# Optimization experiments

Hardware: AMD Instinct MI355X
Metric: run time of the kernel (lower is better)

The kernel has to match this reference:

```python
import jax, jax.numpy as jnp
import numpy as np
from jax import lax

K_SIZE = 5  # dilated_kernel_size


def dcls_kernel(w, p, k=K_SIZE):
    """Build dense (Cout,Cin,k,k) kernel from DCLS v1 bilinear interpolation.
    w: (Cout,Cin,Kc) weights; p: (2,Cout,Cin,Kc) learnable positions."""
    lim = k // 2
    pos = jnp.clip(p, -lim, lim) + lim          # in [0, k-1]
    i = jnp.floor(pos).astype(jnp.int32)
    r = pos - i                                  # bilinear fractions
    Co, Ci, Kc = w.shape
    co = jnp.arange(Co)[:, None, None]
    ci = jnp.arange(Ci)[None, :, None]
    i1, i2 = i[0], i[1]
    r1, r2 = r[0], r[1]
    # scatter into (k+1)x(k+1) grid so i+1 never goes out of bounds, then trim
    K = jnp.zeros((Co, Ci, k + 1, k + 1), w.dtype)
    K = K.at[co, ci, i1,     i2    ].add(w * (1 - r1) * (1 - r2))
    K = K.at[co, ci, i1 + 1, i2    ].add(w * r1 * (1 - r2))
    K = K.at[co, ci, i1,     i2 + 1].add(w * (1 - r1) * r2)
    K = K.at[co, ci, i1 + 1, i2 + 1].add(w * r1 * r2)
    return K[:, :, :k, :k]


def conv2d(x, K, pad):
    return lax.conv_general_dilated(
        x, K, window_strides=(1, 1), padding=[(pad, pad), (pad, pad)],
        dimension_numbers=('NCHW', 'OIHW', 'NCHW'))


def maxpool2(x):
    return lax.reduce_window(x, -jnp.inf, lax.max, (1, 1, 2, 2), (1, 1, 2, 2), 'VALID')


def setup_inputs() -> dict:
    key = jax.random.key(0)
    ks = jax.random.split(key, 12)
    lim = K_SIZE // 2
    B = 4096
    x = jax.random.normal(ks[0], (B, 1, 28, 28), jnp.float32)
    w1 = jax.random.normal(ks[1], (32, 1, 16), jnp.float32) * 0.2
    p1 = jax.random.uniform(ks[2], (2, 32, 1, 16), jnp.float32, -lim, lim)
    b1 = jnp.zeros((32,), jnp.float32)
    w2 = jax.random.normal(ks[3], (64, 32, 32), jnp.float32) * 0.05
    p2 = jax.random.uniform(ks[4], (2, 64, 32, 32), jnp.float32, -lim, lim)
    b2 = jnp.zeros((64,), jnp.float32)
    fc1_w = jax.random.normal(ks[5], (128, 64 * 7 * 7), jnp.float32) * 0.02
    fc1_b = jnp.zeros((128,), jnp.float32)
    fc2_w = jax.random.normal(ks[6], (10, 128), jnp.float32) * 0.08
    fc2_b = jnp.zeros((10,), jnp.float32)
    return dict(x=x, w1=w1, p1=p1, b1=b1, w2=w2, p2=p2, b2=b2,
                fc1_w=fc1_w, fc1_b=fc1_b, fc2_w=fc2_w, fc2_b=fc2_b)


def reference(x, w1, p1, b1, w2, p2, b2, fc1_w, fc1_b, fc2_w, fc2_b):
    h = conv2d(x, dcls_kernel(w1, p1), pad=2) + b1[None, :, None, None]
    h = maxpool2(jax.nn.relu(h))                       # (B,32,14,14)
    h = conv2d(h, dcls_kernel(w2, p2), pad=2) + b2[None, :, None, None]
    h = maxpool2(jax.nn.relu(h))                       # (B,64,7,7)
    h = h.reshape(-1, 64 * 7 * 7)
    h = jax.nn.relu(h @ fc1_w.T + fc1_b)
    return h @ fc2_w.T + fc2_b                         # (B,10)
```

## Files before the change

kernel.cpp:

```cpp
#include <hip/hip_runtime.h>
#include <hip/hip_bf16.h>

typedef __attribute__((ext_vector_type(8))) short short8;
typedef __attribute__((ext_vector_type(4))) short short4v;
typedef __attribute__((ext_vector_type(4))) float float4v;

static __device__ __forceinline__ unsigned short f2bf(float f) {
    unsigned u = __float_as_uint(f);
    unsigned r = (u + 0x7FFF + ((u >> 16) & 1)) >> 16;
    return (unsigned short)r;
}

__global__ __launch_bounds__(256) void prep_all(
    const float* __restrict__ w1, const float* __restrict__ p1,
    const float* __restrict__ w2, const float* __restrict__ p2,
    const float* __restrict__ fc1w,
    unsigned short* __restrict__ K1b,
    unsigned short* __restrict__ Kt,
    unsigned short* __restrict__ w1b) {
    const int blk = blockIdx.x;
    const int t = threadIdx.x;

    if (blk < 8) {
        int cell = blk * 256 + t;
        int co = cell >> 6;
        int k = cell & 63;
        int wr = k >> 3;
        int kx = k & 7;
        float acc = 0.f;
        if (wr < 5 && kx < 5) {
#pragma unroll 8
            for (int kc = 0; kc < 16; ++kc) {
                float wv = w1[co * 16 + kc];
                float pa = p1[co * 16 + kc];
                float pb = p1[512 + co * 16 + kc];
                float pos1 = fminf(fmaxf(pa, -2.f), 2.f) + 2.f;
                float pos2 = fminf(fmaxf(pb, -2.f), 2.f) + 2.f;
                int i1 = (int)floorf(pos1);
                int i2 = (int)floorf(pos2);
                float r1 = pos1 - (float)i1;
                float r2 = pos2 - (float)i2;
                float c = 0.f;
                if (i1 == wr && i2 == kx) c += (1.f - r1) * (1.f - r2);
                if (i1 + 1 == wr && i2 == kx) c += r1 * (1.f - r2);
                if (i1 == wr && i2 + 1 == kx) c += (1.f - r1) * r2;
                if (i1 + 1 == wr && i2 + 1 == kx) c += r1 * r2;
                acc += wv * c;
            }
        }
        K1b[cell] = f2bf(acc);
    } else if (blk < 208) {
        int cell = (blk - 8) * 256 + t;
        int kk = cell >> 11;
        int co = (cell >> 5) & 63;
        int ci = cell & 31;
        int ky = kk / 5;
        int kx = kk - 5 * ky;
        const int base = (co * 32 + ci) * 32;
        float acc = 0.f;
#pragma unroll 8
        for (int kc = 0; kc < 32; ++kc) {
            float wv = w2[base + kc];
            float pa = p2[base + kc];
            float pb = p2[65536 + base + kc];
            float pos1 = fminf(fmaxf(pa, -2.f), 2.f) + 2.f;
            float pos2 = fminf(fmaxf(pb, -2.f), 2.f) + 2.f;
            int i1 = (int)floorf(pos1);
            int i2 = (int)floorf(pos2);
            float r1 = pos1 - (float)i1;
            float r2 = pos2 - (float)i2;
            float c = 0.f;
            if (i1 == ky && i2 == kx) c += (1.f - r1) * (1.f - r2);
            if (i1 + 1 == ky && i2 == kx) c += r1 * (1.f - r2);
            if (i1 == ky && i2 + 1 == kx) c += (1.f - r1) * r2;
            if (i1 + 1 == ky && i2 + 1 == kx) c += r1 * r2;
            acc += wv * c;
        }
        Kt[cell] = f2bf(acc);
    } else {
        int i8 = ((blk - 208) * 256 + t) * 8;
        float4 v0 = *(const float4*)(fc1w + i8);
        float4 v1 = *(const float4*)(fc1w + i8 + 4);
        short8 o = {(short)f2bf(v0.x), (short)f2bf(v0.y), (short)f2bf(v0.z),
                    (short)f2bf(v0.w), (short)f2bf(v1.x), (short)f2bf(v1.y),
                    (short)f2bf(v1.z), (short)f2bf(v1.w)};
        *(short8*)(w1b + i8) = o;
    }
}

__global__ __launch_bounds__(256, 4) void fused_conv_mfma(
    const float* __restrict__ x,
    const unsigned short* __restrict__ K1b,
    const unsigned short* __restrict__ Kt,
    const float* __restrict__ b1,
    const float* __restrict__ b2,
    unsigned short* __restrict__ h2) {
    __shared__ __align__(16) unsigned short h1p[18 * 20 * 40];
    __shared__ __align__(16) unsigned short sm4[4 * 29 * 44];
    __shared__ __align__(16) unsigned short sm_xb[784];

    const int b = blockIdx.x;
    const int tid = threadIdx.x;
    const int lane = tid & 63;
    const int wv = tid >> 6;
    const int n16 = lane & 15;
    const int cig = lane >> 4;

    const int yi = 2 * (n16 >> 3) + ((n16 >> 1) & 1);
    const int xi = 2 * ((n16 >> 2) & 1) + (n16 & 1);
    const int pYo = cig >> 1, pXo = cig & 1;

    for (int t = tid; t < 1800; t += 256) ((uint4*)h1p)[t] = uint4{0, 0, 0, 0};
    {
        const float* xb = x + (size_t)b * 784;
        for (int t = tid; t < 784; t += 256) sm_xb[t] = f2bf(xb[t]);
    }
    __syncthreads();

    if (tid < 116) {
        int s = tid / 29;
        int r = tid - s * 29;
        unsigned short* dst = sm4 + (s * 29 + r) * 44;
        bool rok = r < 28;
#pragma unroll
        for (int g = 0; g < 11; ++g) {
            short4v v;
#pragma unroll
            for (int e = 0; e < 4; ++e) {
                int c = g * 4 + e + s - 4;
                v[e] = (short)((rok && (unsigned)c < 28u) ? sm_xb[r * 28 + c]
                                                          : (unsigned short)0);
            }
            *(short4v*)(dst + g * 4) = v;
        }
    }

    short8 bw[2][2];
    float bias1[2], bias2[4];
#pragma unroll
    for (int cot = 0; cot < 2; ++cot) {
#pragma unroll
        for (int h = 0; h < 2; ++h)
            bw[cot][h] = *(const short8*)(K1b + (cot * 16 + n16) * 64 + h * 32 + cig * 8);
        bias1[cot] = b1[cot * 16 + n16];
    }
#pragma unroll
    for (int cot = 0; cot < 4; ++cot) bias2[cot] = b2[cot * 16 + n16];

    const int s1 = (xi + 2) & 3;
    const int pb1 = (xi + 2) & ~3;
    const unsigned short* a1base = sm4 + s1 * (29 * 44) + pb1;

    __syncthreads();

    for (int i = 0; i < 13; ++i) {
        int t = wv + 4 * i;
        if (t < 49) {
            int tY = t / 7, tX = t - 7 * tY;
            const unsigned short* ab = a1base + 4 * tX;
            int r0 = 4 * tY + yi - 2 + cig;
            int r1 = r0 + 4;
            int rr0 = ((unsigned)r0 < 28u) ? r0 : 28;
            int rr1 = ((unsigned)r1 < 28u) ? r1 : 28;
            short4v lo0 = *(const short4v*)(ab + rr0 * 44);
            short4v hi0 = *(const short4v*)(ab + rr0 * 44 + 4);
            short4v lo1 = *(const short4v*)(ab + rr1 * 44);
            short4v hi1 = *(const short4v*)(ab + rr1 * 44 + 4);
            short8 af0 = {lo0[0], lo0[1], lo0[2], lo0[3], hi0[0], hi0[1], hi0[2], hi0[3]};
            short8 af1 = {lo1[0], lo1[1], lo1[2], lo1[3], hi1[0], hi1[1], hi1[2], hi1[3]};
            int pY = 2 * tY + pYo, pX = 2 * tX + pXo;
#pragma unroll
            for (int cot = 0; cot < 2; ++cot) {
                float4v acc = {0.f, 0.f, 0.f, 0.f};
                acc = __builtin_amdgcn_mfma_f32_16x16x32_bf16(af0, bw[cot][0], acc, 0, 0, 0);
                acc = __builtin_amdgcn_mfma_f32_16x16x32_bf16(af1, bw[cot][1], acc, 0, 0, 0);
                float v = fmaxf(fmaxf(acc[0], acc[1]), fmaxf(acc[2], acc[3]));
                v = fmaxf(v + bias1[cot], 0.f);
                h1p[((pY + 2) * 20 + (pX + 2)) * 40 + cot * 16 + n16] = f2bf(v);
            }
        }
    }
    __syncthreads();

    const unsigned short* Ab[4];
    int pY2[4], pX2[4];
#pragma unroll
    for (int i = 0; i < 4; ++i) {
        int t = wv * 4 + i;
        int tY = t >> 2, tX = t & 3;
        int y2 = 4 * tY + yi;
        y2 = (y2 > 13) ? 13 : y2;
        int x2 = 4 * tX + xi;
        Ab[i] = h1p + (y2 * 20 + x2) * 40 + cig * 8;
        pY2[i] = 2 * tY + pYo;
        pX2[i] = 2 * tX + pXo;
    }

    float4v acc[4][4];
#pragma unroll
    for (int i = 0; i < 4; ++i)
#pragma unroll
        for (int c = 0; c < 4; ++c) acc[i][c] = float4v{0.f, 0.f, 0.f, 0.f};

#pragma unroll
    for (int ky = 0; ky < 5; ++ky) {
#pragma unroll
        for (int kx = 0; kx < 5; ++kx) {
            int kk = ky * 5 + kx;
            short8 wf[4];
#pragma unroll
            for (int cot = 0; cot < 4; ++cot)
                wf[cot] = *(const short8*)(Kt + ((kk * 64 + cot * 16 + n16) * 32 + cig * 8));
#pragma unroll
            for (int i = 0; i < 4; ++i) {
                short8 af = *(const short8*)(Ab[i] + (ky * 20 + kx) * 40);
#pragma unroll
                for (int cot = 0; cot < 4; ++cot)
                    acc[i][cot] = __builtin_amdgcn_mfma_f32_16x16x32_bf16(
                        af, wf[cot], acc[i][cot], 0, 0, 0);
            }
        }
    }

    unsigned short* outb = h2 + (size_t)b * 3136;
#pragma unroll
    for (int i = 0; i < 4; ++i) {
        bool ok = (pY2[i] < 7) & (pX2[i] < 7);
#pragma unroll
        for (int cot = 0; cot < 4; ++cot) {
            float4v a = acc[i][cot];
            float v = fmaxf(fmaxf(a[0], a[1]), fmaxf(a[2], a[3]));
            v = fmaxf(v + bias2[cot], 0.f);
            if (ok)
                outb[(cot * 16 + n16) * 49 + pY2[i] * 7 + pX2[i]] = f2bf(v);
        }
    }
}

__global__ __launch_bounds__(256) void fc1_mfma(
    const unsigned short* __restrict__ A,
    const unsigned short* __restrict__ Wb,
    float* __restrict__ part, size_t PB) {
    const int blk = blockIdx.x;
    const int kh = blk % 7;
    const int m0 = (blk / 7) * 16;
    const int tid = threadIdx.x;
    const int wv = tid >> 6;
    const int lane = tid & 63;
    const int n16 = lane & 15;
    const int cig = lane >> 4;

    const unsigned short* Arow = A + (size_t)(m0 + n16) * 3136 + cig * 8 + kh * 448;
    const unsigned short* W0 = Wb + (size_t)(wv * 32 + n16) * 3136 + cig * 8 + kh * 448;
    const unsigned short* W1 = W0 + 16 * 3136;

    float4v acc0 = {0.f, 0.f, 0.f, 0.f};
    float4v acc1 = {0.f, 0.f, 0.f, 0.f};
#pragma unroll 7
    for (int k = 0; k < 448; k += 32) {
        short8 a = *(const short8*)(Arow + k);
        short8 w0 = *(const short8*)(W0 + k);
        short8 w1 = *(const short8*)(W1 + k);
        acc0 = __builtin_amdgcn_mfma_f32_16x16x32_bf16(a, w0, acc0, 0, 0, 0);
        acc1 = __builtin_amdgcn_mfma_f32_16x16x32_bf16(a, w1, acc1, 0, 0, 0);
    }
    float* o = part + (size_t)kh * PB;
#pragma unroll
    for (int r = 0; r < 4; ++r) {
        int row = m0 + cig * 4 + r;
        o[(size_t)row * 128 + wv * 32 + n16] = acc0[r];
        o[(size_t)row * 128 + wv * 32 + 16 + n16] = acc1[r];
    }
}

__global__ __launch_bounds__(256) void fc2_kernel(
    const float* __restrict__ part, size_t PB,
    const float* __restrict__ fc1b,
    const float* __restrict__ W, const float* __restrict__ bias,
    float* __restrict__ out, int total) {
    __shared__ float smW[10 * 132];
    __shared__ float smB1[128];
    __shared__ float smB[10];
    int t = threadIdx.x;
    for (int i = t; i < 1280; i += 256) {
        int n = i >> 7, k = i & 127;
        smW[n * 132 + k] = W[i];
    }
    if (t < 128) smB1[t] = fc1b[t];
    if (t < 10) smB[t] = bias[t];
    __syncthreads();
    int idx = blockIdx.x * 256 + t;
    if (idx < total) {
        int b = idx / 10;
        int n = idx - b * 10;
        const float4* bb = (const float4*)smB1;
        const float4* wr = (const float4*)(smW + n * 132);
        float acc = smB[n];
#pragma unroll 4
        for (int k = 0; k < 32; ++k) {
            float4 s = *(const float4*)(part + (size_t)b * 128 + 4 * k);
#pragma unroll
            for (int j = 1; j < 7; ++j) {
                float4 pj = *(const float4*)(part + (size_t)j * PB + (size_t)b * 128 + 4 * k);
                s.x += pj.x; s.y += pj.y; s.z += pj.z; s.w += pj.w;
            }
            float4 bv = bb[k];
            float4 w = wr[k];
            acc += fmaxf(s.x + bv.x, 0.f) * w.x + fmaxf(s.y + bv.y, 0.f) * w.y +
                   fmaxf(s.z + bv.z, 0.f) * w.z + fmaxf(s.w + bv.w, 0.f) * w.w;
        }
        out[idx] = acc;
    }
}

extern "C" void kernel_launch(void* const* d_in, const int* in_sizes, int n_in,
                              void* d_out, int out_size, void* d_ws, size_t ws_size,
                              hipStream_t stream) {
    const float* x    = (const float*)d_in[0];
    const float* w1   = (const float*)d_in[1];
    const float* p1   = (const float*)d_in[2];
    const float* b1   = (const float*)d_in[3];
    const float* w2   = (const float*)d_in[4];
    const float* p2   = (const float*)d_in[5];
    const float* b2   = (const float*)d_in[6];
    const float* fc1w = (const float*)d_in[7];
    const float* fc1b = (const float*)d_in[8];
    const float* fc2w = (const float*)d_in[9];
    const float* fc2b = (const float*)d_in[10];
    float* out = (float*)d_out;

    const int B = in_sizes[0] / 784;

    float* ws = (float*)d_ws;
    unsigned short* Kt  = (unsigned short*)ws;
    unsigned short* K1b = (unsigned short*)(ws + 25600);
    unsigned short* w1b = (unsigned short*)(ws + 26624);
    unsigned short* h2b = (unsigned short*)(ws + 227328);
    float* fc1p = ws + 227328 + (size_t)B * 1568;

    prep_all<<<404, 256, 0, stream>>>(w1, p1, w2, p2, fc1w, K1b, Kt, w1b);
    fused_conv_mfma<<<B, 256, 0, stream>>>(x, K1b, Kt, b1, b2, h2b);
    fc1_mfma<<<(B / 16) * 7, 256, 0, stream>>>(h2b, w1b, fc1p, (size_t)B * 128);
    fc2_kernel<<<(B * 10 + 255) / 256, 256, 0, stream>>>(fc1p, (size_t)B * 128,
                                                         fc1b, fc2w, fc2b, out, B * 10);
}
```

Before: 257.5 us.

## Shrink conv LDS, retile conv2, LDS-tile fc1 over 64 rows, split fc2 reduction

The conv kernel trims its LDS buffers (tighter h1 padding, smaller shifted-input rows, input staged in the h1 buffer) to raise occupancy. It also remaps conv2 tiles so only 14 of 16 tile slots do MMA work, and reorders the conv1 weight layout to match. fc1 now stages 64 A rows in shared memory and reuses each weight fragment across 4 M-tiles, which cuts redundant global weight loads. fc2 splits each dot product across 4 lanes and combines them with shuffles for more parallelism. Together these touch every kernel and add index complexity that could introduce layout bugs.

```diff
diff --git a/kernel.cpp b/kernel.cpp
--- a/kernel.cpp
+++ b/kernel.cpp
@@ -23,12 +23,13 @@
 
     if (blk < 8) {
         int cell = blk * 256 + t;
-        int co = cell >> 6;
-        int k = cell & 63;
-        int wr = k >> 3;
+        int half = cell >> 10;
+        int co = (cell >> 5) & 31;
+        int k = cell & 31;
+        int ky = (k >> 3) + 4 * half;
         int kx = k & 7;
         float acc = 0.f;
-        if (wr < 5 && kx < 5) {
+        if (kx < 5 && ky < 5) {
 #pragma unroll 8
             for (int kc = 0; kc < 16; ++kc) {
                 float wv = w1[co * 16 + kc];
@@ -41,10 +42,10 @@
                 float r1 = pos1 - (float)i1;
                 float r2 = pos2 - (float)i2;
                 float c = 0.f;
-                if (i1 == wr && i2 == kx) c += (1.f - r1) * (1.f - r2);
-                if (i1 + 1 == wr && i2 == kx) c += r1 * (1.f - r2);
-                if (i1 == wr && i2 + 1 == kx) c += (1.f - r1) * r2;
-                if (i1 + 1 == wr && i2 + 1 == kx) c += r1 * r2;
+                if (i1 == ky && i2 == kx) c += (1.f - r1) * (1.f - r2);
+                if (i1 + 1 == ky && i2 == kx) c += r1 * (1.f - r2);
+                if (i1 == ky && i2 + 1 == kx) c += (1.f - r1) * r2;
+                if (i1 + 1 == ky && i2 + 1 == kx) c += r1 * r2;
                 acc += wv * c;
             }
         }
@@ -95,9 +96,8 @@
     const float* __restrict__ b1,
     const float* __restrict__ b2,
     unsigned short* __restrict__ h2) {
-    __shared__ __align__(16) unsigned short h1p[18 * 20 * 40];
-    __shared__ __align__(16) unsigned short sm4[4 * 29 * 44];
-    __shared__ __align__(16) unsigned short sm_xb[784];
+    __shared__ __align__(16) unsigned short h1p[18 * 18 * 36];
+    __shared__ __align__(16) unsigned short sm4[4 * 29 * 36];
 
     const int b = blockIdx.x;
     const int tid = threadIdx.x;
@@ -110,20 +110,32 @@
     const int xi = 2 * ((n16 >> 2) & 1) + (n16 & 1);
     const int pYo = cig >> 1, pXo = cig & 1;
 
-    for (int t = tid; t < 1800; t += 256) ((uint4*)h1p)[t] = uint4{0, 0, 0, 0};
+    unsigned short* sm_xb = h1p;
+
     {
         const float* xb = x + (size_t)b * 784;
         for (int t = tid; t < 784; t += 256) sm_xb[t] = f2bf(xb[t]);
     }
+    short8 bw[2][2];
+    float bias1[2], bias2[4];
+#pragma unroll
+    for (int cot = 0; cot < 2; ++cot) {
+#pragma unroll
+        for (int h = 0; h < 2; ++h)
+            bw[cot][h] = *(const short8*)(K1b + (h * 32 + cot * 16 + n16) * 32 + cig * 8);
+        bias1[cot] = b1[cot * 16 + n16];
+    }
+#pragma unroll
+    for (int cot = 0; cot < 4; ++cot) bias2[cot] = b2[cot * 16 + n16];
     __syncthreads();
 
     if (tid < 116) {
         int s = tid / 29;
         int r = tid - s * 29;
-        unsigned short* dst = sm4 + (s * 29 + r) * 44;
+        unsigned short* dst = sm4 + (s * 29 + r) * 36;
         bool rok = r < 28;
 #pragma unroll
-        for (int g = 0; g < 11; ++g) {
+        for (int g = 0; g < 9; ++g) {
             short4v v;
 #pragma unroll
             for (int e = 0; e < 4; ++e) {
@@ -133,106 +145,110 @@
             }
             *(short4v*)(dst + g * 4) = v;
         }
-    }
-
-    short8 bw[2][2];
-    float bias1[2], bias2[4];
-#pragma unroll
-    for (int cot = 0; cot < 2; ++cot) {
-#pragma unroll
-        for (int h = 0; h < 2; ++h)
-            bw[cot][h] = *(const short8*)(K1b + (cot * 16 + n16) * 64 + h * 32 + cig * 8);
-        bias1[cot] = b1[cot * 16 + n16];
-    }
-#pragma unroll
-    for (int cot = 0; cot < 4; ++cot) bias2[cot] = b2[cot * 16 + n16];
-
-    const int s1 = (xi + 2) & 3;
-    const int pb1 = (xi + 2) & ~3;
-    const unsigned short* a1base = sm4 + s1 * (29 * 44) + pb1;
-
-    __syncthreads();
-
-    for (int i = 0; i < 13; ++i) {
-        int t = wv + 4 * i;
-        if (t < 49) {
-            int tY = t / 7, tX = t - 7 * tY;
-            const unsigned short* ab = a1base + 4 * tX;
-            int r0 = 4 * tY + yi - 2 + cig;
-            int r1 = r0 + 4;
-            int rr0 = ((unsigned)r0 < 28u) ? r0 : 28;
-            int rr1 = ((unsigned)r1 < 28u) ? r1 : 28;
-            short4v lo0 = *(const short4v*)(ab + rr0 * 44);
-            short4v hi0 = *(const short4v*)(ab + rr0 * 44 + 4);
-            short4v lo1 = *(const short4v*)(ab + rr1 * 44);
-            short4v hi1 = *(const short4v*)(ab + rr1 * 44 + 4);
-            short8 af0 = {lo0[0], lo0[1], lo0[2], lo0[3], hi0[0], hi0[1], hi0[2], hi0[3]};
-            short8 af1 = {lo1[0], lo1[1], lo1[2], lo1[3], hi1[0], hi1[1], hi1[2], hi1[3]};
-            int pY = 2 * tY + pYo, pX = 2 * tX + pXo;
-#pragma unroll
-            for (int cot = 0; cot < 2; ++cot) {
-                float4v acc = {0.f, 0.f, 0.f, 0.f};
-                acc = __builtin_amdgcn_mfma_f32_16x16x32_bf16(af0, bw[cot][0], acc, 0, 0, 0);
-                acc = __builtin_amdgcn_mfma_f32_16x16x32_bf16(af1, bw[cot][1], acc, 0, 0, 0);
-                float v = fmaxf(fmaxf(acc[0], acc[1]), fmaxf(acc[2], acc[3]));
-                v = fmaxf(v + bias1[cot], 0.f);
-                h1p[((pY + 2) * 20 + (pX + 2)) * 40 + cot * 16 + n16] = f2bf(v);
-            }
-        }
-    }
-    __syncthreads();
-
-    const unsigned short* Ab[4];
-    int pY2[4], pX2[4];
-#pragma unroll
-    for (int i = 0; i < 4; ++i) {
-        int t = wv * 4 + i;
-        int tY = t >> 2, tX = t & 3;
-        int y2 = 4 * tY + yi;
-        y2 = (y2 > 13) ? 13 : y2;
-        int x2 = 4 * tX + xi;
-        Ab[i] = h1p + (y2 * 20 + x2) * 40 + cig * 8;
-        pY2[i] = 2 * tY + pYo;
-        pX2[i] = 2 * tX + pXo;
-    }
-
-    float4v acc[4][4];
-#pragma unroll
-    for (int i = 0; i < 4; ++i)
-#pragma unroll
-        for (int c = 0; c < 4; ++c) acc[i][c] = float4v{0.f, 0.f, 0.f, 0.f};
-
-#pragma unroll
-    for (int ky = 0; ky < 5; ++ky) {
-#pragma unroll
-        for (int kx = 0; kx < 5; ++kx) {
-            int kk = ky * 5 + kx;
-            short8 wf[4];
-#pragma unroll
-            for (int cot = 0; cot < 4; ++cot)
-                wf[cot] = *(const short8*)(Kt + ((kk * 64 + cot * 16 + n16) * 32 + cig * 8));
-#pragma unroll
-            for (int i = 0; i < 4; ++i) {
-                short8 af = *(const short8*)(Ab[i] + (ky * 20 + kx) * 40);
+    } else if (tid >= 120) {
+        for (int i = 98 + (tid - 120); i < 1458; i += 136)
+            ((uint4*)h1p)[i] = uint4{0, 0, 0, 0};
+    }
+    __syncthreads();
+    if (tid < 98) ((uint4*)h1p)[tid] = uint4{0, 0, 0, 0};
+    __syncthreads();
+
+    {
+        const int s1 = (xi + 2) & 3;
+        const int pb1 = (xi + 2) & ~3;
+        const unsigned short* a1base = sm4 + s1 * (29 * 36) + pb1;
+        for (int i = 0; i < 13; ++i) {
+            int t = wv + 4 * i;
+            if (t < 49) {
+                int tY = t / 7, tX = t - 7 * tY;
+                const unsigned short* ab = a1base + 4 * tX;
+                int r0 = 4 * tY + yi - 2 + cig;
+                int r1 = r0 + 4;
+                int rr0 = ((unsigned)r0 < 28u) ? r0 : 28;
+                int rr1 = ((unsigned)r1 < 28u) ? r1 : 28;
+                short4v lo0 = *(const short4v*)(ab + rr0 * 36);
+                short4v hi0 = *(const short4v*)(ab + rr0 * 36 + 4);
+                short4v lo1 = *(const short4v*)(ab + rr1 * 36);
+                short4v hi1 = *(const short4v*)(ab + rr1 * 36 + 4);
+                short8 af0 = {lo0[0], lo0[1], lo0[2], lo0[3], hi0[0], hi0[1], hi0[2], hi0[3]};
+                short8 af1 = {lo1[0], lo1[1], lo1[2], lo1[3], hi1[0], hi1[1], hi1[2], hi1[3]};
+                int pY = 2 * tY + pYo, pX = 2 * tX + pXo;
+#pragma unroll
+                for (int cot = 0; cot < 2; ++cot) {
+                    float4v acc = {0.f, 0.f, 0.f, 0.f};
+                    acc = __builtin_amdgcn_mfma_f32_16x16x32_bf16(af0, bw[cot][0], acc, 0, 0, 0);
+                    acc = __builtin_amdgcn_mfma_f32_16x16x32_bf16(af1, bw[cot][1], acc, 0, 0, 0);
+                    float v = fmaxf(fmaxf(acc[0], acc[1]), fmaxf(acc[2], acc[3]));
+                    v = fmaxf(v + bias1[cot], 0.f);
+                    h1p[((pY + 2) * 18 + (pX + 2)) * 36 + cot * 16 + n16] = f2bf(v);
+                }
+            }
+        }
+    }
+    __syncthreads();
+
+    {
+        const int qx = n16 >> 2, dy = (n16 >> 1) & 1, dxx = n16 & 1;
+        const unsigned short* Ab[4];
+        int tyA[4], pXb[4];
+        bool valid[4];
+#pragma unroll
+        for (int i = 0; i < 4; ++i) {
+            int t = wv + 4 * i;
+            valid[i] = t < 14;
+            int ts = valid[i] ? t : 0;
+            int ty = ts >> 1, sx = ts & 1;
+            int y = 2 * ty + dy;
+            int xc = 8 * sx + 2 * qx + dxx;
+            if (xc > 13) xc = 13;
+            Ab[i] = h1p + (y * 18 + xc) * 36 + cig * 8;
+            tyA[i] = ty;
+            pXb[i] = 4 * sx;
+        }
+
+        float4v acc[4][4];
+#pragma unroll
+        for (int i = 0; i < 4; ++i)
+#pragma unroll
+            for (int c = 0; c < 4; ++c) acc[i][c] = float4v{0.f, 0.f, 0.f, 0.f};
+
+#pragma unroll
+        for (int ky = 0; ky < 5; ++ky) {
+#pragma unroll
+            for (int kx = 0; kx < 5; ++kx) {
+                int kk = ky * 5 + kx;
+                short8 wf[4];
 #pragma unroll
                 for (int cot = 0; cot < 4; ++cot)
-                    acc[i][cot] = __builtin_amdgcn_mfma_f32_16x16x32_bf16(
-                        af, wf[cot], acc[i][cot], 0, 0, 0);
-            }
-        }
-    }
-
-    unsigned short* outb = h2 + (size_t)b * 3136;
-#pragma unroll
-    for (int i = 0; i < 4; ++i) {
-        bool ok = (pY2[i] < 7) & (pX2[i] < 7);
-#pragma unroll
-        for (int cot = 0; cot < 4; ++cot) {
-            float4v a = acc[i][cot];
-            float v = fmaxf(fmaxf(a[0], a[1]), fmaxf(a[2], a[3]));
-            v = fmaxf(v + bias2[cot], 0.f);
-            if (ok)
-                outb[(cot * 16 + n16) * 49 + pY2[i] * 7 + pX2[i]] = f2bf(v);
+                    wf[cot] = *(const short8*)(Kt + ((kk * 64 + cot * 16 + n16) * 32 + cig * 8));
+#pragma unroll
+                for (int i = 0; i < 4; ++i) {
+                    if (valid[i]) {
+                        short8 af = *(const short8*)(Ab[i] + (ky * 18 + kx) * 36);
+#pragma unroll
+                        for (int cot = 0; cot < 4; ++cot)
+                            acc[i][cot] = __builtin_amdgcn_mfma_f32_16x16x32_bf16(
+                                af, wf[cot], acc[i][cot], 0, 0, 0);
+                    }
+                }
+            }
+        }
+
+        unsigned short* outb = h2 + (size_t)b * 3136;
+#pragma unroll
+        for (int i = 0; i < 4; ++i) {
+            if (valid[i]) {
+                int pX = pXb[i] + cig;
+                bool ok = pX < 7;
+#pragma unroll
+                for (int cot = 0; cot < 4; ++cot) {
+                    float4v a = acc[i][cot];
+                    float v = fmaxf(fmaxf(a[0], a[1]), fmaxf(a[2], a[3]));
+                    v = fmaxf(v + bias2[cot], 0.f);
+                    if (ok)
+                        outb[(cot * 16 + n16) * 49 + tyA[i] * 7 + pX] = f2bf(v);
+                }
+            }
         }
     }
 }
@@ -241,43 +257,69 @@
     const unsigned short* __restrict__ A,
     const unsigned short* __restrict__ Wb,
     float* __restrict__ part, size_t PB) {
+    __shared__ __align__(16) unsigned short As[64 * 72];
     const int blk = blockIdx.x;
     const int kh = blk % 7;
-    const int m0 = (blk / 7) * 16;
+    const int m0 = (blk / 7) * 64;
     const int tid = threadIdx.x;
     const int wv = tid >> 6;
     const int lane = tid & 63;
     const int n16 = lane & 15;
     const int cig = lane >> 4;
 
-    const unsigned short* Arow = A + (size_t)(m0 + n16) * 3136 + cig * 8 + kh * 448;
-    const unsigned short* W0 = Wb + (size_t)(wv * 32 + n16) * 3136 + cig * 8 + kh * 448;
-    const unsigned short* W1 = W0 + 16 * 3136;
-
-    float4v acc0 = {0.f, 0.f, 0.f, 0.f};
-    float4v acc1 = {0.f, 0.f, 0.f, 0.f};
-#pragma unroll 7
-    for (int k = 0; k < 448; k += 32) {
-        short8 a = *(const short8*)(Arow + k);
-        short8 w0 = *(const short8*)(W0 + k);
-        short8 w1 = *(const short8*)(W1 + k);
-        acc0 = __builtin_amdgcn_mfma_f32_16x16x32_bf16(a, w0, acc0, 0, 0, 0);
-        acc1 = __builtin_amdgcn_mfma_f32_16x16x32_bf16(a, w1, acc1, 0, 0, 0);
+    float4v acc[4][2];
+#pragma unroll
+    for (int mt = 0; mt < 4; ++mt)
+#pragma unroll
+        for (int j = 0; j < 2; ++j) acc[mt][j] = float4v{0.f, 0.f, 0.f, 0.f};
+
+    for (int it = 0; it < 7; ++it) {
+        int k0 = kh * 448 + it * 64;
+        __syncthreads();
+#pragma unroll
+        for (int i = 0; i < 2; ++i) {
+            int p = tid + 256 * i;
+            int r = p >> 3, ko = (p & 7) * 8;
+            *(short8*)(As + r * 72 + ko) =
+                *(const short8*)(A + (size_t)(m0 + r) * 3136 + k0 + ko);
+        }
+        __syncthreads();
+#pragma unroll
+        for (int h = 0; h < 2; ++h) {
+            short8 af[4];
+#pragma unroll
+            for (int mt = 0; mt < 4; ++mt)
+                af[mt] = *(const short8*)(As + (mt * 16 + n16) * 72 + h * 32 + cig * 8);
+            short8 wf[2];
+#pragma unroll
+            for (int j = 0; j < 2; ++j)
+                wf[j] = *(const short8*)(Wb + (size_t)((wv * 2 + j) * 16 + n16) * 3136 +
+                                         k0 + h * 32 + cig * 8);
+#pragma unroll
+            for (int mt = 0; mt < 4; ++mt)
+#pragma unroll
+                for (int j = 0; j < 2; ++j)
+                    acc[mt][j] = __builtin_amdgcn_mfma_f32_16x16x32_bf16(
+                        af[mt], wf[j], acc[mt][j], 0, 0, 0);
+        }
     }
     float* o = part + (size_t)kh * PB;
 #pragma unroll
-    for (int r = 0; r < 4; ++r) {
-        int row = m0 + cig * 4 + r;
-        o[(size_t)row * 128 + wv * 32 + n16] = acc0[r];
-        o[(size_t)row * 128 + wv * 32 + 16 + n16] = acc1[r];
-    }
+    for (int mt = 0; mt < 4; ++mt)
+#pragma unroll
+        for (int j = 0; j < 2; ++j)
+#pragma unroll
+            for (int r = 0; r < 4; ++r) {
+                int row = m0 + mt * 16 + cig * 4 + r;
+                o[(size_t)row * 128 + (wv * 2 + j) * 16 + n16] = acc[mt][j][r];
+            }
 }
 
 __global__ __launch_bounds__(256) void fc2_kernel(
     const float* __restrict__ part, size_t PB,
     const float* __restrict__ fc1b,
     const float* __restrict__ W, const float* __restrict__ bias,
-    float* __restrict__ out, int total) {
+    float* __restrict__ out, int total4) {
     __shared__ float smW[10 * 132];
     __shared__ float smB1[128];
     __shared__ float smB[10];
@@ -290,26 +332,31 @@
     if (t < 10) smB[t] = bias[t];
     __syncthreads();
     int idx = blockIdx.x * 256 + t;
-    if (idx < total) {
-        int b = idx / 10;
-        int n = idx - b * 10;
-        const float4* bb = (const float4*)smB1;
-        const float4* wr = (const float4*)(smW + n * 132);
-        float acc = smB[n];
-#pragma unroll 4
-        for (int k = 0; k < 32; ++k) {
-            float4 s = *(const float4*)(part + (size_t)b * 128 + 4 * k);
-#pragma unroll
-            for (int j = 1; j < 7; ++j) {
-                float4 pj = *(const float4*)(part + (size_t)j * PB + (size_t)b * 128 + 4 * k);
+    if (idx < total4) {
+        int j = idx >> 2;
+        int q = idx & 3;
+        int b = j / 10;
+        int n = j - b * 10;
+        const float* pb = part + (size_t)b * 128 + q * 32;
+        const float4* bb = (const float4*)(smB1 + q * 32);
+        const float4* wr = (const float4*)(smW + n * 132 + q * 32);
+        float acc = 0.f;
+#pragma unroll
+        for (int c = 0; c < 8; ++c) {
+            float4 s = *(const float4*)(pb + 4 * c);
+#pragma unroll
+            for (int jj = 1; jj < 7; ++jj) {
+                float4 pj = *(const float4*)(pb + (size_t)jj * PB + 4 * c);
                 s.x += pj.x; s.y += pj.y; s.z += pj.z; s.w += pj.w;
             }
-            float4 bv = bb[k];
-            float4 w = wr[k];
+            float4 bv = bb[c];
+            float4 w = wr[c];
             acc += fmaxf(s.x + bv.x, 0.f) * w.x + fmaxf(s.y + bv.y, 0.f) * w.y +
                    fmaxf(s.z + bv.z, 0.f) * w.z + fmaxf(s.w + bv.w, 0.f) * w.w;
         }
-        out[idx] = acc;
+        acc += __shfl_xor(acc, 1);
+        acc += __shfl_xor(acc, 2);
+        if (q == 0) out[j] = acc + smB[n];
     }
 }
 
@@ -340,7 +387,7 @@
 
     prep_all<<<404, 256, 0, stream>>>(w1, p1, w2, p2, fc1w, K1b, Kt, w1b);
     fused_conv_mfma<<<B, 256, 0, stream>>>(x, K1b, Kt, b1, b2, h2b);
-    fc1_mfma<<<(B / 16) * 7, 256, 0, stream>>>(h2b, w1b, fc1p, (size_t)B * 128);
-    fc2_kernel<<<(B * 10 + 255) / 256, 256, 0, stream>>>(fc1p, (size_t)B * 128,
-                                                         fc1b, fc2w, fc2b, out, B * 10);
-}
+    fc1_mfma<<<(B / 64) * 7, 256, 0, stream>>>(h2b, w1b, fc1p, (size_t)B * 128);
+    fc2_kernel<<<(B * 10 * 4 + 255) / 256, 256, 0, stream>>>(
+        fc1p, (size_t)B * 128, fc1b, fc2w, fc2b, out, B * 10 * 4);
+}
```

After: 300.3 us. 1.17x slower.
